# Kernel optimization log

Hardware: AMD Instinct MI355X
Metric: run time of the kernel (lower is better)

Reference implementation:

```python
import jax, jax.numpy as jnp
import numpy as np

N_NODES = 100000
N_EDGES = 1600000
D_IN = 128
HID = 128
OUT = 128
N_GRAPHS = 512
BN_EPS = 1e-5


def setup_inputs() -> dict:
    key = jax.random.key(0)
    ks = jax.random.split(key, 24)
    s = 0.05
    inp = {
        "x": jax.random.normal(ks[0], (N_NODES, D_IN), dtype=jnp.float32),
        "edge_index": jax.random.randint(ks[1], (2, N_EDGES), 0, N_NODES, dtype=jnp.int32),
        "batch": jnp.sort(jax.random.randint(ks[2], (N_NODES,), 0, N_GRAPHS, dtype=jnp.int32)),
        # GIN MLP 1
        "W1a": jax.random.normal(ks[3], (D_IN, HID)) * s, "b1a": jnp.zeros((HID,)),
        "W1b": jax.random.normal(ks[4], (HID, HID)) * s, "b1b": jnp.zeros((HID,)),
        "g1": jnp.ones((HID,)), "be1": jnp.zeros((HID,)),
        # GIN MLP 2
        "W2a": jax.random.normal(ks[5], (HID, HID)) * s, "b2a": jnp.zeros((HID,)),
        "W2b": jax.random.normal(ks[6], (HID, HID)) * s, "b2b": jnp.zeros((HID,)),
        "g2": jnp.ones((HID,)), "be2": jnp.zeros((HID,)),
        # GIN MLP 3
        "W3a": jax.random.normal(ks[7], (HID, HID)) * s, "b3a": jnp.zeros((HID,)),
        "W3b": jax.random.normal(ks[8], (HID, HID)) * s, "b3b": jnp.zeros((HID,)),
        "g3": jnp.ones((HID,)), "be3": jnp.zeros((HID,)),
        # final linear
        "Wl": jax.random.normal(ks[9], (3 * HID, OUT)) * s, "bl": jnp.zeros((OUT,)),
    }
    return inp


def _gin(x, edge_index, Wa, ba, Wb, bb):
    # GINConv with eps=0: nn(x_i + sum_{j->i} x_j)
    msgs = x[edge_index[0]]                                  # [E, d] gather
    agg = jax.ops.segment_sum(msgs, edge_index[1], num_segments=N_NODES)
    h = x + agg
    return jax.nn.relu(h @ Wa + ba) @ Wb + bb


def _bn_relu(h, g, b):
    # BatchNorm1d in training mode: biased batch stats over node axis
    m = jnp.mean(h, axis=0)
    v = jnp.mean(jnp.square(h - m), axis=0)
    return jax.nn.relu((h - m) * jax.lax.rsqrt(v + BN_EPS) * g + b)


def _mean_pool(h, batch):
    sums = jax.ops.segment_sum(h, batch, num_segments=N_GRAPHS)       # [G, d]
    cnt = jax.ops.segment_sum(jnp.ones((h.shape[0],), h.dtype), batch,
                              num_segments=N_GRAPHS)
    return sums / jnp.maximum(cnt, 1.0)[:, None]


def reference(x, edge_index, batch,
              W1a, b1a, W1b, b1b, g1, be1,
              W2a, b2a, W2b, b2b, g2, be2,
              W3a, b3a, W3b, b3b, g3, be3,
              Wl, bl):
    h1 = _bn_relu(_gin(x, edge_index, W1a, b1a, W1b, b1b), g1, be1)
    h2 = _bn_relu(_gin(h1, edge_index, W2a, b2a, W2b, b2b), g2, be2)
    h3 = _bn_relu(_gin(h2, edge_index, W3a, b3a, W3b, b3b), g3, be3)
    hf = jnp.concatenate([_mean_pool(h1, batch), _mean_pool(h2, batch),
                          _mean_pool(h3, batch)], axis=1)             # [G, 3H]
    z = hf @ Wl + bl                                                   # [G, O]
    norm = jnp.linalg.norm(z, axis=1, keepdims=True)
    return z / jnp.maximum(norm, 1e-12)
```

## Files before the change

kernel.cpp:

```cpp
#include <hip/hip_runtime.h>
#include <hip/hip_bf16.h>
#include <hip/hip_fp16.h>

#define N_NODES 100000
#define N_EDGES 1600000
#define N_GRAPHS 512
#define BN_EPS 1e-5f
#define NBKT 196
#define PART_CHUNK 4096

typedef float f32x4 __attribute__((ext_vector_type(4)));
typedef short s16x8 __attribute__((ext_vector_type(8)));

__device__ inline ushort f2bf(float f) {
    union { float f; unsigned u; } v; v.f = f;
    unsigned u = v.u;
    unsigned r = (u + 0x7FFFu + ((u >> 16) & 1u)) >> 16;
    return (ushort)r;
}
__device__ inline float bf2f(ushort h) {
    union { unsigned u; float f; } v; v.u = ((unsigned)h) << 16;
    return v.f;
}


__global__ __launch_bounds__(256) void k_bcnt(const int4* __restrict__ dst4, int* __restrict__ bcnt, int E4) {
    __shared__ int h[NBKT];
    int tid = threadIdx.x;
    for (int i = tid; i < NBKT; i += 256) h[i] = 0;
    __syncthreads();
    for (int t = blockIdx.x * 256 + tid; t < E4; t += gridDim.x * 256) {
        int4 d = dst4[t];
        atomicAdd(&h[d.x >> 9], 1);
        atomicAdd(&h[d.y >> 9], 1);
        atomicAdd(&h[d.z >> 9], 1);
        atomicAdd(&h[d.w >> 9], 1);
    }
    __syncthreads();
    for (int i = tid; i < NBKT; i += 256) {
        int v = h[i];
        if (v) atomicAdd(&bcnt[i], v);
    }
}


__global__ __launch_bounds__(256) void k_bscan(const int* __restrict__ bcnt, int* __restrict__ bbase,
                                               int* __restrict__ gcur) {
    __shared__ int buf[256];
    int tid = threadIdx.x;
    int v = (tid < NBKT) ? bcnt[tid] : 0;
    buf[tid] = v;
    __syncthreads();
    for (int st = 1; st < 256; st <<= 1) {
        int t = (tid >= st) ? buf[tid - st] : 0;
        __syncthreads();
        buf[tid] += t;
        __syncthreads();
    }
    int excl = buf[tid] - v;
    if (tid < NBKT) {
        bbase[tid] = excl;
        gcur[tid] = excl;
    }
    if (tid == NBKT - 1) bbase[NBKT] = excl + v;
}


__global__ __launch_bounds__(256) void k_gstart(const int* __restrict__ batch, int* __restrict__ gcnt, int N) {
    int g = blockIdx.x * 256 + threadIdx.x;
    if (g >= N_GRAPHS) return;
    auto lb = [&](int key) {
        int lo = 0, hi = N;
        while (lo < hi) {
            int mid = (lo + hi) >> 1;
            if (batch[mid] < key) lo = mid + 1; else hi = mid;
        }
        return lo;
    };
    gcnt[g] = lb(g + 1) - lb(g);
}


__global__ __launch_bounds__(256) void k_x2h(const float4* __restrict__ x4, uint4* __restrict__ xh, int n8) {
    int i = blockIdx.x * 256 + threadIdx.x;
    if (i >= n8) return;
    float4 a = x4[2 * i], b = x4[2 * i + 1];
    union { uint4 u4; __half h[8]; } cv;
    cv.h[0] = __float2half(a.x); cv.h[1] = __float2half(a.y);
    cv.h[2] = __float2half(a.z); cv.h[3] = __float2half(a.w);
    cv.h[4] = __float2half(b.x); cv.h[5] = __float2half(b.y);
    cv.h[6] = __float2half(b.z); cv.h[7] = __float2half(b.w);
    xh[i] = cv.u4;
}


__global__ __launch_bounds__(256) void k_part(const int* __restrict__ esrc, const int* __restrict__ edst,
                                              int* __restrict__ gcur, unsigned* __restrict__ ebuf, int E) {
    __shared__ int cnt[256], base[256], scn[256];
    __shared__ unsigned ebufL[PART_CHUNK];
    __shared__ int gposL[PART_CHUNK];
    int tid = threadIdx.x;
    int e0 = blockIdx.x * PART_CHUNK;
    int nv = min(PART_CHUNK, E - e0);
    int src[16], dst[16];
    cnt[tid] = 0;
    __syncthreads();
    const int4* s4 = (const int4*)(esrc + e0);
    const int4* d4 = (const int4*)(edst + e0);
    int n4 = nv >> 2;
#pragma unroll
    for (int t = 0; t < 4; ++t) {
        int i4 = t * 256 + tid;
        if (i4 < n4) {
            int4 s = s4[i4];
            int4 d = d4[i4];
            src[t * 4 + 0] = s.x; src[t * 4 + 1] = s.y; src[t * 4 + 2] = s.z; src[t * 4 + 3] = s.w;
            dst[t * 4 + 0] = d.x; dst[t * 4 + 1] = d.y; dst[t * 4 + 2] = d.z; dst[t * 4 + 3] = d.w;
            atomicAdd(&cnt[d.x >> 9], 1);
            atomicAdd(&cnt[d.y >> 9], 1);
            atomicAdd(&cnt[d.z >> 9], 1);
            atomicAdd(&cnt[d.w >> 9], 1);
        } else {
            dst[t * 4 + 0] = -1; dst[t * 4 + 1] = -1; dst[t * 4 + 2] = -1; dst[t * 4 + 3] = -1;
            src[t * 4 + 0] = 0; src[t * 4 + 1] = 0; src[t * 4 + 2] = 0; src[t * 4 + 3] = 0;
        }
    }
    __syncthreads();
    int c = cnt[tid];
    if (tid < NBKT) base[tid] = atomicAdd(&gcur[tid], c);
    scn[tid] = c;
    __syncthreads();
    for (int st = 1; st < 256; st <<= 1) {
        int t = (tid >= st) ? scn[tid - st] : 0;
        __syncthreads();
        scn[tid] += t;
        __syncthreads();
    }
    scn[tid] -= c;
    __syncthreads();
    cnt[tid] = 0;
    __syncthreads();
#pragma unroll
    for (int t = 0; t < 16; ++t) {
        if (dst[t] >= 0) {
            int b = dst[t] >> 9;
            int r = atomicAdd(&cnt[b], 1);
            int s = scn[b] + r;
            ebufL[s] = (((unsigned)(dst[t] & 511)) << 17) | (unsigned)src[t];
            gposL[s] = base[b] + r;
        }
    }
    __syncthreads();
    for (int s = tid; s < nv; s += 256) ebuf[gposL[s]] = ebufL[s];
}


__global__ __launch_bounds__(256) void k_bucket(const unsigned* __restrict__ ebuf, const int* __restrict__ bbase,
                                                int* __restrict__ off, int* __restrict__ srcs, int N) {
    __shared__ int degL[512];
    __shared__ int s2[256];
    int b = blockIdx.x;
    int n0 = b << 9;
    int nn = min(512, N - n0);
    int tid = threadIdx.x;
    for (int i = tid; i < nn; i += 256) degL[i] = 0;
    __syncthreads();
    int e0 = bbase[b], e1 = bbase[b + 1];
    for (int i = e0 + tid; i < e1; i += 256) atomicAdd(&degL[ebuf[i] >> 17], 1);
    __syncthreads();
    int a0 = (2 * tid < nn) ? degL[2 * tid] : 0;
    int a1 = (2 * tid + 1 < nn) ? degL[2 * tid + 1] : 0;
    int ps = a0 + a1;
    s2[tid] = ps;
    __syncthreads();
    for (int st = 1; st < 256; st <<= 1) {
        int t = (tid >= st) ? s2[tid - st] : 0;
        __syncthreads();
        s2[tid] += t;
        __syncthreads();
    }
    int excl = s2[tid] - ps;
    if (2 * tid < nn) { off[n0 + 2 * tid] = e0 + excl; degL[2 * tid] = e0 + excl; }
    if (2 * tid + 1 < nn) { off[n0 + 2 * tid + 1] = e0 + excl + a0; degL[2 * tid + 1] = e0 + excl + a0; }
    if (b == NBKT - 1 && tid == 0) off[N] = e1;
    __syncthreads();
    for (int i = e0 + tid; i < e1; i += 256) {
        unsigned p = ebuf[i];
        int dl = (int)(p >> 17);
        int pos = atomicAdd(&degL[dl], 1);
        srcs[pos] = (int)(p & 0x1FFFFu);
    }
}


struct W6 { const float* w[6]; };

__global__ __launch_bounds__(256) void k_packw6(W6 ws6, ushort* __restrict__ pk) {
    int m = blockIdx.x >> 6;
    int p = (blockIdx.x & 63) * 256 + threadIdx.x;
    const float* W = ws6.w[m];
    ushort* o = pk + (size_t)m * 32768;
    int j = p & 7, l = (p >> 3) & 63, n = (p >> 9) & 7, kc = p >> 12;
    int row = kc * 32 + ((l >> 4) & 3) * 8 + j;
    int col = n * 16 + (l & 15);
    float wv = W[row * 128 + col];
    ushort hi = f2bf(wv);
    ushort lo = f2bf(wv - bf2f(hi));
    o[p] = hi;
    o[16384 + p] = lo;
}


template <bool HASBN>
__global__ __launch_bounds__(256) void k_agg_h(const __half* __restrict__ Xh, float* __restrict__ T,
        const int* __restrict__ off, const int* __restrict__ srcs,
        const float* __restrict__ stats, const float* __restrict__ gamma, const float* __restrict__ beta,
        int N) {
    int gid = blockIdx.x * 256 + threadIdx.x;
    int w = gid >> 6;
    int lane = threadIdx.x & 63;
    int q = lane >> 4;
    int lc = lane & 15;
    int node = w * 4 + q;
    if (node >= N) return;

    float g[8], b[8];
    if (HASBN) {
        float invN = 1.0f / (float)N;
        float4 m1a = ((const float4*)stats)[lc * 2];
        float4 m1b = ((const float4*)stats)[lc * 2 + 1];
        float4 m2a = ((const float4*)stats)[32 + lc * 2];
        float4 m2b = ((const float4*)stats)[32 + lc * 2 + 1];
        float4 ga = ((const float4*)gamma)[lc * 2];
        float4 gb = ((const float4*)gamma)[lc * 2 + 1];
        float4 ba = ((const float4*)beta)[lc * 2];
        float4 bb = ((const float4*)beta)[lc * 2 + 1];
        float m1[8] = {m1a.x, m1a.y, m1a.z, m1a.w, m1b.x, m1b.y, m1b.z, m1b.w};
        float m2[8] = {m2a.x, m2a.y, m2a.z, m2a.w, m2b.x, m2b.y, m2b.z, m2b.w};
        float gm[8] = {ga.x, ga.y, ga.z, ga.w, gb.x, gb.y, gb.z, gb.w};
        float bt[8] = {ba.x, ba.y, ba.z, ba.w, bb.x, bb.y, bb.z, bb.w};
#pragma unroll
        for (int t = 0; t < 8; ++t) {
            float mean = m1[t] * invN;
            float var = m2[t] * invN - mean * mean;
            float r = rsqrtf(var + BN_EPS);
            g[t] = gm[t] * r;
            b[t] = bt[t] - mean * g[t];
        }
    }

    const uint4* X16 = (const uint4*)Xh;
    float acc[8];
    union { uint4 u4; __half h[8]; } cv;

    auto addrow = [&](uint4 raw) {
        union { uint4 u4; __half h[8]; } c2;
        c2.u4 = raw;
#pragma unroll
        for (int t = 0; t < 8; ++t) {
            float v = __half2float(c2.h[t]);
            if (HASBN) v = fmaxf(fmaf(v, g[t], b[t]), 0.f);
            acc[t] += v;
        }
    };

    cv.u4 = X16[(size_t)node * 16 + lc];
#pragma unroll
    for (int t = 0; t < 8; ++t) {
        float v = __half2float(cv.h[t]);
        if (HASBN) v = fmaxf(fmaf(v, g[t], b[t]), 0.f);
        acc[t] = v;
    }

    int s = off[node], e = off[node + 1];
    int j = s;
    for (; j + 7 < e; j += 8) {
        int u0 = srcs[j], u1 = srcs[j + 1], u2 = srcs[j + 2], u3 = srcs[j + 3];
        int u4 = srcs[j + 4], u5 = srcs[j + 5], u6 = srcs[j + 6], u7 = srcs[j + 7];
        uint4 r0 = X16[(size_t)u0 * 16 + lc];
        uint4 r1 = X16[(size_t)u1 * 16 + lc];
        uint4 r2 = X16[(size_t)u2 * 16 + lc];
        uint4 r3 = X16[(size_t)u3 * 16 + lc];
        uint4 r4 = X16[(size_t)u4 * 16 + lc];
        uint4 r5 = X16[(size_t)u5 * 16 + lc];
        uint4 r6 = X16[(size_t)u6 * 16 + lc];
        uint4 r7 = X16[(size_t)u7 * 16 + lc];
        addrow(r0); addrow(r1); addrow(r2); addrow(r3);
        addrow(r4); addrow(r5); addrow(r6); addrow(r7);
    }
    for (; j < e; ++j) addrow(X16[(size_t)srcs[j] * 16 + lc]);

    float4 o0 = make_float4(acc[0], acc[1], acc[2], acc[3]);
    float4 o1 = make_float4(acc[4], acc[5], acc[6], acc[7]);
    ((float4*)T)[(size_t)node * 32 + lc * 2] = o0;
    ((float4*)T)[(size_t)node * 32 + lc * 2 + 1] = o1;
}


__global__ __launch_bounds__(256, 2) void k_mlp_pair(const float* __restrict__ A, __half* __restrict__ out,
        const ushort* __restrict__ pk1, const float* __restrict__ b1,
        const ushort* __restrict__ pk2, const float* __restrict__ b2,
        float* __restrict__ stats, int N) {
    __shared__ float tile[4 * 32 * 128];
    int tid = threadIdx.x;
    int wid = tid >> 6, l = tid & 63;
    int lr = l & 15, lg = l >> 4;
    int r0 = blockIdx.x * 128 + wid * 32;
    int wbase = wid * 32 * 128;

    const f32x4* A4 = (const f32x4*)A;
    const s16x8* B1 = (const s16x8*)pk1;
    const s16x8* B2 = (const s16x8*)pk2;

    f32x4 acc[2][8];
#pragma unroll
    for (int m = 0; m < 2; ++m)
#pragma unroll
        for (int n = 0; n < 8; ++n) acc[m][n] = (f32x4){0.f, 0.f, 0.f, 0.f};

#pragma unroll
    for (int kc = 0; kc < 4; ++kc) {
        s16x8 ahi[2], alo[2];
#pragma unroll
        for (int m = 0; m < 2; ++m) {
            int row = min(r0 + m * 16 + lr, N - 1);
            f32x4 v0 = A4[(size_t)row * 32 + kc * 8 + lg * 2];
            f32x4 v1 = A4[(size_t)row * 32 + kc * 8 + lg * 2 + 1];
            float f[8] = {v0.x, v0.y, v0.z, v0.w, v1.x, v1.y, v1.z, v1.w};
#pragma unroll
            for (int j = 0; j < 8; ++j) {
                ushort hi = f2bf(f[j]);
                ahi[m][j] = (short)hi;
                alo[m][j] = (short)f2bf(f[j] - bf2f(hi));
            }
        }
#pragma unroll
        for (int n = 0; n < 8; ++n) {
            int fi = (kc * 8 + n) * 64 + l;
            s16x8 bhi = B1[fi];
            s16x8 blo = B1[2048 + fi];
#pragma unroll
            for (int m = 0; m < 2; ++m) {
                acc[m][n] = __builtin_amdgcn_mfma_f32_16x16x32_bf16(ahi[m], bhi, acc[m][n], 0, 0, 0);
                acc[m][n] = __builtin_amdgcn_mfma_f32_16x16x32_bf16(alo[m], bhi, acc[m][n], 0, 0, 0);
                acc[m][n] = __builtin_amdgcn_mfma_f32_16x16x32_bf16(ahi[m], blo, acc[m][n], 0, 0, 0);
            }
        }
    }

#pragma unroll
    for (int n = 0; n < 8; ++n) {
        float bv = b1[n * 16 + lr];
        int c4 = n * 4 + (lr >> 2);
        int e = lr & 3;
#pragma unroll
        for (int m = 0; m < 2; ++m) {
#pragma unroll
            for (int i = 0; i < 4; ++i) {
                int row = m * 16 + lg * 4 + i;
                float v = fmaxf(acc[m][n][i] + bv, 0.f);
                tile[wbase + row * 128 + ((c4 ^ (row & 7)) << 2) + e] = v;
            }
        }
    }
    __syncthreads();

#pragma unroll
    for (int m = 0; m < 2; ++m)
#pragma unroll
        for (int n = 0; n < 8; ++n) acc[m][n] = (f32x4){0.f, 0.f, 0.f, 0.f};

#pragma unroll
    for (int kc = 0; kc < 4; ++kc) {
        s16x8 ahi[2], alo[2];
#pragma unroll
        for (int m = 0; m < 2; ++m) {
            int row = m * 16 + lr;
            float f[8];
#pragma unroll
            for (int h = 0; h < 2; ++h) {
                int k4 = kc * 8 + lg * 2 + h;
                f32x4 v = *(const f32x4*)&tile[wbase + row * 128 + ((k4 ^ (row & 7)) << 2)];
                f[h * 4 + 0] = v.x; f[h * 4 + 1] = v.y; f[h * 4 + 2] = v.z; f[h * 4 + 3] = v.w;
            }
#pragma unroll
            for (int j = 0; j < 8; ++j) {
                ushort hi = f2bf(f[j]);
                ahi[m][j] = (short)hi;
                alo[m][j] = (short)f2bf(f[j] - bf2f(hi));
            }
        }
#pragma unroll
        for (int n = 0; n < 8; ++n) {
            int fi = (kc * 8 + n) * 64 + l;
            s16x8 bhi = B2[fi];
            s16x8 blo = B2[2048 + fi];
#pragma unroll
            for (int m = 0; m < 2; ++m) {
                acc[m][n] = __builtin_amdgcn_mfma_f32_16x16x32_bf16(ahi[m], bhi, acc[m][n], 0, 0, 0);
                acc[m][n] = __builtin_amdgcn_mfma_f32_16x16x32_bf16(alo[m], bhi, acc[m][n], 0, 0, 0);
                acc[m][n] = __builtin_amdgcn_mfma_f32_16x16x32_bf16(ahi[m], blo, acc[m][n], 0, 0, 0);
            }
        }
    }
    __syncthreads();

    float s1[8], s2[8];
#pragma unroll
    for (int n = 0; n < 8; ++n) { s1[n] = 0.f; s2[n] = 0.f; }

#pragma unroll
    for (int n = 0; n < 8; ++n) {
        float bv = b2[n * 16 + lr];
#pragma unroll
        for (int m = 0; m < 2; ++m) {
#pragma unroll
            for (int i = 0; i < 4; ++i) {
                int r = r0 + m * 16 + lg * 4 + i;
                if (r < N) {
                    float v = acc[m][n][i] + bv;
                    s1[n] += v;
                    s2[n] += v * v;
                    out[(size_t)r * 128 + n * 16 + lr] = __float2half(v);
                }
            }
        }
    }

    float* ls = tile;
#pragma unroll
    for (int n = 0; n < 8; ++n) {
        float a = s1[n], b = s2[n];
        a += __shfl_xor(a, 16, 64); a += __shfl_xor(a, 32, 64);
        b += __shfl_xor(b, 16, 64); b += __shfl_xor(b, 32, 64);
        if (lg == 0) {
            ls[wid * 256 + n * 16 + lr] = a;
            ls[wid * 256 + 128 + n * 16 + lr] = b;
        }
    }
    __syncthreads();
    float t = ls[tid] + ls[256 + tid] + ls[512 + tid] + ls[768 + tid];
    atomicAdd(&stats[tid], t);
}


__global__ __launch_bounds__(128) void k_pool(const __half* __restrict__ h, const float* __restrict__ stats,
                                              const float* __restrict__ gamma, const float* __restrict__ beta,
                                              const int* __restrict__ batch, float* __restrict__ pool,
                                              int loff, int N) {
    int c = threadIdx.x;
    const float invN = 1.0f / (float)N;
    float mean = stats[c] * invN;
    float var = stats[128 + c] * invN - mean * mean;
    float rstd = rsqrtf(var + BN_EPS);
    float gsc = gamma[c] * rstd;
    float bs = beta[c] - mean * gsc;

    int r0 = blockIdx.x * 64;
    int r1 = min(r0 + 64, N);
    float acc = 0.f;
    int curg = -1;
    for (int r = r0; r < r1; ++r) {
        float v = __half2float(h[(size_t)r * 128 + c]);
        float hv = fmaxf(fmaf(v, gsc, bs), 0.f);
        int g = batch[r];
        if (g != curg) {
            if (curg >= 0) atomicAdd(&pool[(size_t)curg * 384 + loff + c], acc);
            curg = g;
            acc = hv;
        } else {
            acc += hv;
        }
    }
    if (curg >= 0) atomicAdd(&pool[(size_t)curg * 384 + loff + c], acc);
}


__global__ __launch_bounds__(128) void k_final(const float* __restrict__ pool, const int* __restrict__ gcnt,
                                               const float* __restrict__ Wl, const float* __restrict__ bl,
                                               float* __restrict__ out) {
    __shared__ float sh[384];
    __shared__ float red[128];
    int g = blockIdx.x;
    int tid = threadIdx.x;
    float inv = 1.0f / fmaxf((float)gcnt[g], 1.0f);
    for (int t = tid; t < 384; t += 128) sh[t] = pool[(size_t)g * 384 + t] * inv;
    __syncthreads();
    float acc = bl[tid];
    for (int k = 0; k < 384; ++k) acc = fmaf(sh[k], Wl[(size_t)k * 128 + tid], acc);
    red[tid] = acc * acc;
    __syncthreads();
    for (int s = 64; s > 0; s >>= 1) {
        if (tid < s) red[tid] += red[tid + s];
        __syncthreads();
    }
    float norm = sqrtf(red[0]);
    float scale = 1.0f / fmaxf(norm, 1e-12f);
    out[(size_t)g * 128 + tid] = acc * scale;
}


extern "C" void kernel_launch(void* const* d_in, const int* in_sizes, int n_in,
                              void* d_out, int out_size, void* d_ws, size_t ws_size,
                              hipStream_t stream) {
    const float* x = (const float*)d_in[0];
    const int* edge_index = (const int*)d_in[1];
    const int* batch = (const int*)d_in[2];
    const float* Wa[3] = {(const float*)d_in[3], (const float*)d_in[9], (const float*)d_in[15]};
    const float* ba[3] = {(const float*)d_in[4], (const float*)d_in[10], (const float*)d_in[16]};
    const float* Wb[3] = {(const float*)d_in[5], (const float*)d_in[11], (const float*)d_in[17]};
    const float* bb[3] = {(const float*)d_in[6], (const float*)d_in[12], (const float*)d_in[18]};
    const float* gm[3] = {(const float*)d_in[7], (const float*)d_in[13], (const float*)d_in[19]};
    const float* be[3] = {(const float*)d_in[8], (const float*)d_in[14], (const float*)d_in[20]};
    const float* Wl = (const float*)d_in[21];
    const float* bl = (const float*)d_in[22];
    float* out = (float*)d_out;

    const int N = N_NODES, E = N_EDGES, G = N_GRAPHS;
    const int* e_src = edge_index;
    const int* e_dst = edge_index + E;

    char* ws = (char*)d_ws;
    size_t o = 0;
    auto alloc = [&](size_t bytes) -> char* {
        char* p = ws + o;
        o = (o + bytes + 255) & ~(size_t)255;
        return p;
    };
    int* off = (int*)alloc((size_t)(N + 1) * 4);
    int* srcs = (int*)alloc((size_t)E * 4);
    int* gcnt = (int*)alloc((size_t)G * 4);
    int* bcnt = (int*)alloc(256 * 4);
    int* bbase = (int*)alloc(256 * 4);
    int* gcur = (int*)alloc(256 * 4);
    float* stats = (float*)alloc(3 * 256 * 4);
    ushort* wpk = (ushort*)alloc(6 * 32768 * 2);
    float* pool = (float*)alloc((size_t)G * 384 * 4);
    float* T = (float*)alloc((size_t)N * 128 * 4);
    __half* Ha = (__half*)alloc((size_t)N * 128 * 2);
    __half* Hb = (__half*)alloc((size_t)N * 128 * 2);
    unsigned* ebuf = (unsigned*)T;
    (void)ws_size;

    hipMemsetAsync(bcnt, 0, 256 * 4, stream);
    hipMemsetAsync(stats, 0, 3 * 256 * 4, stream);
    hipMemsetAsync(pool, 0, (size_t)G * 384 * 4, stream);

    const int E4 = E / 4;

    k_bcnt<<<256, 256, 0, stream>>>((const int4*)e_dst, bcnt, E4);
    k_bscan<<<1, 256, 0, stream>>>(bcnt, bbase, gcur);
    k_gstart<<<2, 256, 0, stream>>>(batch, gcnt, N);
    k_part<<<(E + PART_CHUNK - 1) / PART_CHUNK, 256, 0, stream>>>(e_src, e_dst, gcur, ebuf, E);
    k_bucket<<<NBKT, 256, 0, stream>>>(ebuf, bbase, off, srcs, N);

    const int n8 = N * 128 / 8;
    k_x2h<<<(n8 + 255) / 256, 256, 0, stream>>>((const float4*)x, (uint4*)Ha, n8);

    W6 w6;
    w6.w[0] = Wa[0]; w6.w[1] = Wb[0]; w6.w[2] = Wa[1];
    w6.w[3] = Wb[1]; w6.w[4] = Wa[2]; w6.w[5] = Wb[2];
    k_packw6<<<384, 256, 0, stream>>>(w6, wpk);

    const int aggBlocks = ((N + 3) / 4 * 64 + 255) / 256;
    const int mlpBlocks = (N + 127) / 128;
    const int poolBlocks = (N + 63) / 64;

    __half* hin[3] = {Ha, Hb, Ha};
    __half* hout[3] = {Hb, Ha, Hb};
    for (int l = 0; l < 3; ++l) {
        float* statsl = stats + l * 256;
        if (l == 0)
            k_agg_h<false><<<aggBlocks, 256, 0, stream>>>(hin[l], T, off, srcs, nullptr, nullptr, nullptr, N);
        else
            k_agg_h<true><<<aggBlocks, 256, 0, stream>>>(hin[l], T, off, srcs, stats + (l - 1) * 256,
                                                         gm[l - 1], be[l - 1], N);
        k_mlp_pair<<<mlpBlocks, 256, 0, stream>>>(T, hout[l], wpk + (size_t)(2 * l) * 32768, ba[l],
                                                  wpk + (size_t)(2 * l + 1) * 32768, bb[l], statsl, N);
        k_pool<<<poolBlocks, 128, 0, stream>>>(hout[l], statsl, gm[l], be[l], batch, pool, l * 128, N);
    }

    k_final<<<G, 128, 0, stream>>>(pool, gcnt, Wl, bl, out);
}
```

Before: 557.5 us.

## Materialize BN+ReLU activations in pool kernel so aggregation gathers plain halves

```diff
diff --git a/kernel.cpp b/kernel.cpp
--- a/kernel.cpp
+++ b/kernel.cpp
@@ -211,11 +211,8 @@
 }
 
 
-template <bool HASBN>
-__global__ __launch_bounds__(256) void k_agg_h(const __half* __restrict__ Xh, float* __restrict__ T,
-        const int* __restrict__ off, const int* __restrict__ srcs,
-        const float* __restrict__ stats, const float* __restrict__ gamma, const float* __restrict__ beta,
-        int N) {
+__global__ __launch_bounds__(256) void k_agg(const __half* __restrict__ Xh, float* __restrict__ T,
+                                             const int* __restrict__ off, const int* __restrict__ srcs, int N) {
     int gid = blockIdx.x * 256 + threadIdx.x;
     int w = gid >> 6;
     int lane = threadIdx.x & 63;
@@ -224,52 +221,14 @@
     int node = w * 4 + q;
     if (node >= N) return;
 
-    float g[8], b[8];
-    if (HASBN) {
-        float invN = 1.0f / (float)N;
-        float4 m1a = ((const float4*)stats)[lc * 2];
-        float4 m1b = ((const float4*)stats)[lc * 2 + 1];
-        float4 m2a = ((const float4*)stats)[32 + lc * 2];
-        float4 m2b = ((const float4*)stats)[32 + lc * 2 + 1];
-        float4 ga = ((const float4*)gamma)[lc * 2];
-        float4 gb = ((const float4*)gamma)[lc * 2 + 1];
-        float4 ba = ((const float4*)beta)[lc * 2];
-        float4 bb = ((const float4*)beta)[lc * 2 + 1];
-        float m1[8] = {m1a.x, m1a.y, m1a.z, m1a.w, m1b.x, m1b.y, m1b.z, m1b.w};
-        float m2[8] = {m2a.x, m2a.y, m2a.z, m2a.w, m2b.x, m2b.y, m2b.z, m2b.w};
-        float gm[8] = {ga.x, ga.y, ga.z, ga.w, gb.x, gb.y, gb.z, gb.w};
-        float bt[8] = {ba.x, ba.y, ba.z, ba.w, bb.x, bb.y, bb.z, bb.w};
-#pragma unroll
-        for (int t = 0; t < 8; ++t) {
-            float mean = m1[t] * invN;
-            float var = m2[t] * invN - mean * mean;
-            float r = rsqrtf(var + BN_EPS);
-            g[t] = gm[t] * r;
-            b[t] = bt[t] - mean * g[t];
-        }
-    }
-
     const uint4* X16 = (const uint4*)Xh;
-    float acc[8];
-    union { uint4 u4; __half h[8]; } cv;
-
-    auto addrow = [&](uint4 raw) {
-        union { uint4 u4; __half h[8]; } c2;
-        c2.u4 = raw;
-#pragma unroll
-        for (int t = 0; t < 8; ++t) {
-            float v = __half2float(c2.h[t]);
-            if (HASBN) v = fmaxf(fmaf(v, g[t], b[t]), 0.f);
-            acc[t] += v;
-        }
-    };
-
-    cv.u4 = X16[(size_t)node * 16 + lc];
-#pragma unroll
-    for (int t = 0; t < 8; ++t) {
-        float v = __half2float(cv.h[t]);
-        if (HASBN) v = fmaxf(fmaf(v, g[t], b[t]), 0.f);
-        acc[t] = v;
+    union U { uint4 u4; __half2 h[4]; };
+
+    float2 acc[4];
+    {
+        U r; r.u4 = X16[(size_t)node * 16 + lc];
+#pragma unroll
+        for (int k = 0; k < 4; ++k) acc[k] = __half22float2(r.h[k]);
     }
 
     int s = off[node], e = off[node + 1];
@@ -277,21 +236,41 @@
     for (; j + 7 < e; j += 8) {
         int u0 = srcs[j], u1 = srcs[j + 1], u2 = srcs[j + 2], u3 = srcs[j + 3];
         int u4 = srcs[j + 4], u5 = srcs[j + 5], u6 = srcs[j + 6], u7 = srcs[j + 7];
-        uint4 r0 = X16[(size_t)u0 * 16 + lc];
-        uint4 r1 = X16[(size_t)u1 * 16 + lc];
-        uint4 r2 = X16[(size_t)u2 * 16 + lc];
-        uint4 r3 = X16[(size_t)u3 * 16 + lc];
-        uint4 r4 = X16[(size_t)u4 * 16 + lc];
-        uint4 r5 = X16[(size_t)u5 * 16 + lc];
-        uint4 r6 = X16[(size_t)u6 * 16 + lc];
-        uint4 r7 = X16[(size_t)u7 * 16 + lc];
-        addrow(r0); addrow(r1); addrow(r2); addrow(r3);
-        addrow(r4); addrow(r5); addrow(r6); addrow(r7);
-    }
-    for (; j < e; ++j) addrow(X16[(size_t)srcs[j] * 16 + lc]);
-
-    float4 o0 = make_float4(acc[0], acc[1], acc[2], acc[3]);
-    float4 o1 = make_float4(acc[4], acc[5], acc[6], acc[7]);
+        U r0, r1, r2, r3, r4, r5, r6, r7;
+        r0.u4 = X16[(size_t)u0 * 16 + lc];
+        r1.u4 = X16[(size_t)u1 * 16 + lc];
+        r2.u4 = X16[(size_t)u2 * 16 + lc];
+        r3.u4 = X16[(size_t)u3 * 16 + lc];
+        r4.u4 = X16[(size_t)u4 * 16 + lc];
+        r5.u4 = X16[(size_t)u5 * 16 + lc];
+        r6.u4 = X16[(size_t)u6 * 16 + lc];
+        r7.u4 = X16[(size_t)u7 * 16 + lc];
+#pragma unroll
+        for (int k = 0; k < 4; ++k) {
+            float2 f0 = __half22float2(r0.h[k]), f1 = __half22float2(r1.h[k]);
+            float2 f2 = __half22float2(r2.h[k]), f3 = __half22float2(r3.h[k]);
+            float2 f4 = __half22float2(r4.h[k]), f5 = __half22float2(r5.h[k]);
+            float2 f6 = __half22float2(r6.h[k]), f7 = __half22float2(r7.h[k]);
+            float2 a01 = make_float2(f0.x + f1.x, f0.y + f1.y);
+            float2 a23 = make_float2(f2.x + f3.x, f2.y + f3.y);
+            float2 a45 = make_float2(f4.x + f5.x, f4.y + f5.y);
+            float2 a67 = make_float2(f6.x + f7.x, f6.y + f7.y);
+            acc[k].x += (a01.x + a23.x) + (a45.x + a67.x);
+            acc[k].y += (a01.y + a23.y) + (a45.y + a67.y);
+        }
+    }
+    for (; j < e; ++j) {
+        U r; r.u4 = X16[(size_t)srcs[j] * 16 + lc];
+#pragma unroll
+        for (int k = 0; k < 4; ++k) {
+            float2 f = __half22float2(r.h[k]);
+            acc[k].x += f.x;
+            acc[k].y += f.y;
+        }
+    }
+
+    float4 o0 = make_float4(acc[0].x, acc[0].y, acc[1].x, acc[1].y);
+    float4 o1 = make_float4(acc[2].x, acc[2].y, acc[3].x, acc[3].y);
     ((float4*)T)[(size_t)node * 32 + lc * 2] = o0;
     ((float4*)T)[(size_t)node * 32 + lc * 2 + 1] = o1;
 }
@@ -444,10 +423,11 @@
 }
 
 
-__global__ __launch_bounds__(128) void k_pool(const __half* __restrict__ h, const float* __restrict__ stats,
-                                              const float* __restrict__ gamma, const float* __restrict__ beta,
-                                              const int* __restrict__ batch, float* __restrict__ pool,
-                                              int loff, int N) {
+__global__ __launch_bounds__(128) void k_bnpool(const __half* __restrict__ h, __half* __restrict__ hp,
+                                                const float* __restrict__ stats,
+                                                const float* __restrict__ gamma, const float* __restrict__ beta,
+                                                const int* __restrict__ batch, float* __restrict__ pool,
+                                                int loff, int N) {
     int c = threadIdx.x;
     const float invN = 1.0f / (float)N;
     float mean = stats[c] * invN;
@@ -463,6 +443,7 @@
     for (int r = r0; r < r1; ++r) {
         float v = __half2float(h[(size_t)r * 128 + c]);
         float hv = fmaxf(fmaf(v, gsc, bs), 0.f);
+        hp[(size_t)r * 128 + c] = __float2half(hv);
         int g = batch[r];
         if (g != curg) {
             if (curg >= 0) atomicAdd(&pool[(size_t)curg * 384 + loff + c], acc);
@@ -537,8 +518,8 @@
     ushort* wpk = (ushort*)alloc(6 * 32768 * 2);
     float* pool = (float*)alloc((size_t)G * 384 * 4);
     float* T = (float*)alloc((size_t)N * 128 * 4);
-    __half* Ha = (__half*)alloc((size_t)N * 128 * 2);
-    __half* Hb = (__half*)alloc((size_t)N * 128 * 2);
+    __half* B0 = (__half*)alloc((size_t)N * 128 * 2);
+    __half* B1 = (__half*)alloc((size_t)N * 128 * 2);
     unsigned* ebuf = (unsigned*)T;
     (void)ws_size;
 
@@ -555,7 +536,7 @@
     k_bucket<<<NBKT, 256, 0, stream>>>(ebuf, bbase, off, srcs, N);
 
     const int n8 = N * 128 / 8;
-    k_x2h<<<(n8 + 255) / 256, 256, 0, stream>>>((const float4*)x, (uint4*)Ha, n8);
+    k_x2h<<<(n8 + 255) / 256, 256, 0, stream>>>((const float4*)x, (uint4*)B0, n8);
 
     W6 w6;
     w6.w[0] = Wa[0]; w6.w[1] = Wb[0]; w6.w[2] = Wa[1];
@@ -564,20 +545,14 @@
 
     const int aggBlocks = ((N + 3) / 4 * 64 + 255) / 256;
     const int mlpBlocks = (N + 127) / 128;
-    const int poolBlocks = (N + 63) / 64;
-
-    __half* hin[3] = {Ha, Hb, Ha};
-    __half* hout[3] = {Hb, Ha, Hb};
+    const int bnBlocks = (N + 63) / 64;
+
     for (int l = 0; l < 3; ++l) {
         float* statsl = stats + l * 256;
-        if (l == 0)
-            k_agg_h<false><<<aggBlocks, 256, 0, stream>>>(hin[l], T, off, srcs, nullptr, nullptr, nullptr, N);
-        else
-            k_agg_h<true><<<aggBlocks, 256, 0, stream>>>(hin[l], T, off, srcs, stats + (l - 1) * 256,
-                                                         gm[l - 1], be[l - 1], N);
-        k_mlp_pair<<<mlpBlocks, 256, 0, stream>>>(T, hout[l], wpk + (size_t)(2 * l) * 32768, ba[l],
+        k_agg<<<aggBlocks, 256, 0, stream>>>(B0, T, off, srcs, N);
+        k_mlp_pair<<<mlpBlocks, 256, 0, stream>>>(T, B1, wpk + (size_t)(2 * l) * 32768, ba[l],
                                                   wpk + (size_t)(2 * l + 1) * 32768, bb[l], statsl, N);
-        k_pool<<<poolBlocks, 128, 0, stream>>>(hout[l], statsl, gm[l], be[l], batch, pool, l * 128, N);
+        k_bnpool<<<bnBlocks, 128, 0, stream>>>(B1, B0, statsl, gm[l], be[l], batch, pool, l * 128, N);
     }
 
     k_final<<<G, 128, 0, stream>>>(pool, gcnt, Wl, bl, out);
```

After: 558.5 us. Within noise of the previous version (+0.2%).
